# Kernel tuning notes

Measured on AMD Instinct MI355X. Metric: run time of the kernel, lower is better.

Reference implementation:

```python
import jax, jax.numpy as jnp
import numpy as np

NUM_HEAD = 8
MSA_DIM = 256
PAIR_DIM = 128
KEY_DIM = MSA_DIM // NUM_HEAD  # 32 per-head dim
LN_EPS = 1e-5


def _layernorm(x, scale, offset):
    mu = jnp.mean(x, axis=-1, keepdims=True)
    var = jnp.var(x, axis=-1, keepdims=True)
    return (x - mu) * jax.lax.rsqrt(var + LN_EPS) * scale + offset


def setup_inputs() -> dict:
    key = jax.random.key(0)
    ks = jax.random.split(key, 16)
    S, R = 256, 256  # num sequences, num residues
    inp = {
        "msa_act": jax.random.normal(ks[0], (S, R, MSA_DIM), dtype=jnp.float32),
        "msa_mask": jnp.ones((S, R), dtype=jnp.int32),
        "pair_act": jax.random.normal(ks[1], (R, R, PAIR_DIM), dtype=jnp.float32),
        # LayerNorm params
        "qn_scale": jax.random.normal(ks[2], (MSA_DIM,), dtype=jnp.float32) * 0.02 + 1.0,
        "qn_offset": jax.random.normal(ks[3], (MSA_DIM,), dtype=jnp.float32) * 0.02,
        "pn_scale": jax.random.normal(ks[4], (PAIR_DIM,), dtype=jnp.float32) * 0.02 + 1.0,
        "pn_offset": jax.random.normal(ks[5], (PAIR_DIM,), dtype=jnp.float32) * 0.02,
        # pair-bias projection
        "feat_2d_weights": jax.random.normal(ks[6], (PAIR_DIM, NUM_HEAD), dtype=jnp.float32) * 0.1,
        # attention params
        "q_weights": jax.random.normal(ks[7], (MSA_DIM, NUM_HEAD, KEY_DIM), dtype=jnp.float32) * 0.05,
        "k_weights": jax.random.normal(ks[8], (MSA_DIM, NUM_HEAD, KEY_DIM), dtype=jnp.float32) * 0.05,
        "v_weights": jax.random.normal(ks[9], (MSA_DIM, NUM_HEAD, KEY_DIM), dtype=jnp.float32) * 0.05,
        "o_weights": jax.random.normal(ks[10], (NUM_HEAD, KEY_DIM, MSA_DIM), dtype=jnp.float32) * 0.05,
        "o_bias": jnp.zeros((MSA_DIM,), dtype=jnp.float32),
        "gating_w": jax.random.normal(ks[11], (MSA_DIM, NUM_HEAD, KEY_DIM), dtype=jnp.float32) * 0.05,
        "gating_b": jnp.ones((NUM_HEAD, KEY_DIM), dtype=jnp.float32),
    }
    return inp


def reference(msa_act, msa_mask, pair_act, qn_scale, qn_offset, pn_scale, pn_offset,
              feat_2d_weights, q_weights, k_weights, v_weights, o_weights, o_bias,
              gating_w, gating_b):
    # mask bias: [S, 1, 1, R]
    bias = (1e9 * (msa_mask.astype(jnp.float32) - 1.0))[:, None, None, :]
    m = _layernorm(msa_act, qn_scale, qn_offset)            # [S, R, C]
    p = _layernorm(pair_act, pn_scale, pn_offset)           # [R, R, Cz]
    nonbatched_bias = jnp.einsum('qkc,ch->hqk', p, feat_2d_weights)  # [H, R, R]

    q = jnp.einsum('bqa,ahc->bqhc', m, q_weights) * (KEY_DIM ** -0.5)
    k = jnp.einsum('bka,ahc->bkhc', m, k_weights)
    v = jnp.einsum('bka,ahc->bkhc', m, v_weights)
    logits = jnp.einsum('bqhc,bkhc->bhqk', q, k) + bias + nonbatched_bias[None]
    weights = jax.nn.softmax(logits, axis=-1)
    weighted_avg = jnp.einsum('bhqk,bkhc->bqhc', weights, v)

    gate = jax.nn.sigmoid(jnp.einsum('bqc,chv->bqhv', m, gating_w) + gating_b)
    weighted_avg = weighted_avg * gate

    out = jnp.einsum('bqhc,hco->bqo', weighted_avg, o_weights) + o_bias
    return out
```

## Files before the change

kernel.cpp:

```cpp
#include <hip/hip_runtime.h>
#include <hip/hip_bf16.h>
#include <stdint.h>


typedef unsigned short u16;
typedef unsigned int   u32;
typedef __attribute__((ext_vector_type(8))) short bf16x8;
typedef __attribute__((ext_vector_type(4))) float f32x4;

__device__ __forceinline__ float bf2f(u16 u){ union { u32 i; float f; } v; v.i = ((u32)u)<<16; return v.f; }
__device__ __forceinline__ u16 f2bf(float f){
  union { float f; u32 i; } v; v.f = f; u32 x = v.i;
  return (u16)((x + 0x7fffu + ((x>>16)&1u)) >> 16);
}
__device__ __forceinline__ u32 pk2(float a, float b){ return (u32)f2bf(a) | ((u32)f2bf(b) << 16); }

__device__ __forceinline__ void gl_lds16(const void* g, void* l){
  __builtin_amdgcn_global_load_lds(
    reinterpret_cast<const __attribute__((address_space(1))) unsigned int*>(reinterpret_cast<uintptr_t>(g)),
    reinterpret_cast<__attribute__((address_space(3))) unsigned int*>(reinterpret_cast<uintptr_t>(l)),
    16, 0, 0);
}

__global__ __launch_bounds__(256) void k_ln_msa(
    const float* __restrict__ x, const float* __restrict__ sc,
    const float* __restrict__ of, u16* __restrict__ mo)
{
  const int lane = threadIdx.x & 63;
  const int row  = (blockIdx.x << 2) + (threadIdx.x >> 6);
  float4 v = ((const float4*)(x + (size_t)row * 256))[lane];
  float s  = v.x + v.y + v.z + v.w;
  float s2 = v.x*v.x + v.y*v.y + v.z*v.z + v.w*v.w;
  #pragma unroll
  for (int o = 32; o > 0; o >>= 1){ s += __shfl_xor(s, o); s2 += __shfl_xor(s2, o); }
  const float mu = s * (1.0f/256.0f);
  const float rs = rsqrtf(s2 * (1.0f/256.0f) - mu*mu + 1e-5f);
  float4 scv = ((const float4*)sc)[lane];
  float4 ofv = ((const float4*)of)[lane];
  u32 p0 = pk2((v.x-mu)*rs*scv.x + ofv.x, (v.y-mu)*rs*scv.y + ofv.y);
  u32 p1 = pk2((v.z-mu)*rs*scv.z + ofv.z, (v.w-mu)*rs*scv.w + ofv.w);
  ((uint2*)(mo + (size_t)row * 256))[lane] = make_uint2(p0, p1);
}

__global__ __launch_bounds__(256) void k_ln_pair(
    const float* __restrict__ p, const float* __restrict__ sc,
    const float* __restrict__ of, const float* __restrict__ w2d,
    float* __restrict__ nb)
{
  const int lane = threadIdx.x & 63;
  const int row  = (blockIdx.x << 2) + (threadIdx.x >> 6);
  float2 v = ((const float2*)(p + (size_t)row * 128))[lane];
  float s = v.x + v.y, s2 = v.x*v.x + v.y*v.y;
  #pragma unroll
  for (int o = 32; o > 0; o >>= 1){ s += __shfl_xor(s, o); s2 += __shfl_xor(s2, o); }
  const float mu = s * (1.0f/128.0f);
  const float rs = rsqrtf(s2 * (1.0f/128.0f) - mu*mu + 1e-5f);
  const int c0 = lane * 2;
  const float y0 = (v.x - mu) * rs * sc[c0]     + of[c0];
  const float y1 = (v.y - mu) * rs * sc[c0 + 1] + of[c0 + 1];
  const float4* w0 = (const float4*)(w2d + c0 * 8);
  const float4* w1 = (const float4*)(w2d + (c0 + 1) * 8);
  float4 a0 = w0[0], b0 = w0[1], a1 = w1[0], b1 = w1[1];
  float ph[8];
  ph[0] = y0*a0.x + y1*a1.x; ph[1] = y0*a0.y + y1*a1.y;
  ph[2] = y0*a0.z + y1*a1.z; ph[3] = y0*a0.w + y1*a1.w;
  ph[4] = y0*b0.x + y1*b1.x; ph[5] = y0*b0.y + y1*b1.y;
  ph[6] = y0*b0.z + y1*b1.z; ph[7] = y0*b0.w + y1*b1.w;
  #pragma unroll
  for (int o = 32; o > 0; o >>= 1){
    #pragma unroll
    for (int hh = 0; hh < 8; hh++) ph[hh] += __shfl_xor(ph[hh], o);
  }
  if (lane == 0){
    #pragma unroll
    for (int hh = 0; hh < 8; hh++) nb[(size_t)hh * 65536 + row] = ph[hh];
  }
}

__global__ __launch_bounds__(256) void k_cast(
    const float* __restrict__ qw, const float* __restrict__ kw,
    const float* __restrict__ vw, const float* __restrict__ gw,
    const float* __restrict__ ow, u16* __restrict__ wT)
{
  const int mt = blockIdx.x >> 4;
  const float* src = (mt == 0) ? qw : (mt == 1) ? kw : (mt == 2) ? vw : (mt == 3) ? gw : ow;
  u16* dst = wT + mt * 65536;
  const int tid = threadIdx.x;
  const int n  = ((blockIdx.x & 15) << 4) + (tid & 15);
  const int kc = tid >> 4;
  float v[16];
  #pragma unroll
  for (int kk = 0; kk < 16; kk++) v[kk] = src[(kc*16 + kk)*256 + n];
  #pragma unroll
  for (int p = 0; p < 8; p++)
    *(u32*)&dst[n*256 + kc*16 + 2*p] = pk2(v[2*p], v[2*p+1]);
}

__global__ __launch_bounds__(256) void k_qkvg(
    const u16* __restrict__ m, const u16* __restrict__ wT, const float* __restrict__ gb,
    u16* __restrict__ qo, u16* __restrict__ ko, u16* __restrict__ vTo, u16* __restrict__ go)
{
  __shared__ __align__(16) u16 As[8192];
  __shared__ __align__(16) u16 Bs[8192];
  const int tid = threadIdx.x;
  const int w = tid >> 6, lane = tid & 63, g = lane >> 4, q16 = lane & 15;
  const int by = blockIdx.x & 7, bx = blockIdx.x >> 3;
  const int row0  = bx << 7;
  const int mat   = by >> 1;
  const int ncol0 = (by & 1) << 7;
  const u16* Wt = wT + mat * 65536;
  const int wr = w >> 1, wc = w & 1;

  const int rA  = ((tid >> 7) << 4) + (tid & 15);
  const int kgA = (tid >> 4) & 7;

  const f32x4 z4 = {0.f, 0.f, 0.f, 0.f};
  f32x4 acc[4][4];
  #pragma unroll
  for (int i = 0; i < 4; i++)
    #pragma unroll
    for (int j = 0; j < 4; j++) acc[i][j] = z4;

  #pragma unroll 1
  for (int ks = 0; ks < 4; ks++){
    const int k0 = ks << 6;
    #pragma unroll
    for (int c = 0; c < 4; c++){
      gl_lds16(m  + (size_t)(row0  + rA + c*32)*256 + k0 + kgA*8,
               (char*)As + c*4096 + w*1024);
      gl_lds16(Wt + (size_t)(ncol0 + rA + c*32)*256 + k0 + kgA*8,
               (char*)Bs + c*4096 + w*1024);
    }
    __syncthreads();
    #pragma unroll
    for (int kk = 0; kk < 2; kk++){
      bf16x8 af[4], bfr[4];
      #pragma unroll
      for (int i = 0; i < 4; i++){
        af[i]  = *(const bf16x8*)((const char*)As + (wr*4+i)*2048 + (kk*4+g)*256 + q16*16);
        bfr[i] = *(const bf16x8*)((const char*)Bs + (wc*4+i)*2048 + (kk*4+g)*256 + q16*16);
      }
      #pragma unroll
      for (int i = 0; i < 4; i++)
        #pragma unroll
        for (int j = 0; j < 4; j++)
          acc[i][j] = __builtin_amdgcn_mfma_f32_16x16x32_bf16(af[i], bfr[j], acc[i][j], 0, 0, 0);
    }
    __syncthreads();
  }

  const int b  = bx >> 1;
  const int rb = (row0 & 255) + wr*64 + 4*g;
  const int cb0 = ncol0 + wc*64 + q16;

  if (mat == 2){
    #pragma unroll
    for (int i = 0; i < 4; i++){
      const int r = rb + i*16;
      #pragma unroll
      for (int j = 0; j < 4; j++){
        const int col = cb0 + j*16;
        const int hh = col >> 5, cc = col & 31;
        u16* base = vTo + (size_t)(b*8 + hh)*8192 + cc*256 + r;
        *(u32*)base       = pk2(acc[i][j][0], acc[i][j][1]);
        *(u32*)(base + 2) = pk2(acc[i][j][2], acc[i][j][3]);
      }
    }
  } else {
    u16* O = (mat == 0) ? qo : (mat == 1) ? ko : go;
    #pragma unroll
    for (int i = 0; i < 4; i++){
      #pragma unroll
      for (int j = 0; j < 4; j++){
        const int col = cb0 + j*16;
        const int hh = col >> 5, cc = col & 31;
        f32x4 a = acc[i][j];
        if (mat == 0) a *= 0.17677669529663687f;
        #pragma unroll
        for (int v = 0; v < 4; v++){
          float x = a[v];
          if (mat == 3) x = 1.0f / (1.0f + __expf(-(x + gb[col])));
          O[(size_t)((b*8 + hh)*256 + rb + i*16 + v)*32 + cc] = f2bf(x);
        }
      }
    }
  }
}

__global__ __launch_bounds__(512, 4) void k_attn(
    const u16* __restrict__ qp, const u16* __restrict__ kp, const u16* __restrict__ vTp,
    const u16* __restrict__ gp, const int* __restrict__ mask, const float* __restrict__ nb,
    u16* __restrict__ gwa)
{
  __shared__ __align__(16) u16 Ksh[8192];
  __shared__ __align__(16) u16 Vsh[8192];
  __shared__ __align__(16) u16 Pb[8][2048];
  __shared__ float maskb[256];
  const int tid = threadIdx.x;
  const int w = tid >> 6, lane = tid & 63, g = lane >> 4, q16 = lane & 15;
  const int blk = blockIdx.x, b = blk >> 3, h = blk & 7;
  const size_t tb = (size_t)blk * 8192;

  #pragma unroll
  for (int c = 0; c < 2; c++){
    gl_lds16(kp  + tb + (size_t)((c*8 + w)*16 + q16)*32 + g*8,
             (char*)Ksh + c*8192 + w*1024);
    gl_lds16(vTp + tb + (size_t)(c*16 + q16)*256 + (w*4 + g)*8,
             (char*)Vsh + c*8192 + w*1024);
  }
  if (tid < 256) maskb[tid] = 1e9f * ((float)mask[b*256 + tid] - 1.0f);
  __syncthreads();

  const float* nbh = nb + (size_t)h * 65536;
  const f32x4 z4 = {0.f,0.f,0.f,0.f};
  u16* pb = Pb[w];
  const int rsw = (g ^ (q16 & 3)) << 4;

  #pragma unroll 1
  for (int jj = 0; jj < 2; jj++){
    const int q = w*32 + jj*16 + q16;
    const bf16x8 qf = *(const bf16x8*)(qp + tb + (size_t)q*32 + g*8);
    f32x4 O0 = z4, O1 = z4;
    float l = 0.f, mrun = -3.0e38f;

    #pragma unroll 1
    for (int hh = 0; hh < 2; hh++){
      f32x4 S[8];
      #pragma unroll
      for (int n8 = 0; n8 < 8; n8++){
        const bf16x8 kf = *(const bf16x8*)((const char*)Ksh + (hh*8+n8)*1024 + g*256 + q16*16);
        S[n8] = __builtin_amdgcn_mfma_f32_16x16x32_bf16(kf, qf, z4, 0, 0, 0);
      }
      float hmax = -3.0e38f;
      #pragma unroll
      for (int n8 = 0; n8 < 8; n8++){
        const f32x4 nbv = *(const f32x4*)(nbh + (size_t)q*256 + (hh*8+n8)*16 + 4*g);
        const f32x4 mbv = *(const f32x4*)&maskb[(hh*8+n8)*16 + 4*g];
        S[n8] += nbv + mbv;
        hmax = fmaxf(hmax, fmaxf(fmaxf(S[n8][0],S[n8][1]), fmaxf(S[n8][2],S[n8][3])));
      }
      hmax = fmaxf(hmax, __shfl_xor(hmax, 16));
      hmax = fmaxf(hmax, __shfl_xor(hmax, 32));
      const float mnew = fmaxf(mrun, hmax);
      const float fsc = __expf(mrun - mnew);
      l *= fsc; O0 *= fsc; O1 *= fsc; mrun = mnew;

      u32 cpk[8], dpk[8];
      #pragma unroll
      for (int n8 = 0; n8 < 8; n8++){
        const float p0 = __expf(S[n8][0]-mnew), p1 = __expf(S[n8][1]-mnew);
        const float p2 = __expf(S[n8][2]-mnew), p3 = __expf(S[n8][3]-mnew);
        l += (p0+p1)+(p2+p3);
        cpk[n8] = pk2(p0,p1); dpk[n8] = pk2(p2,p3);
      }
      #pragma unroll
      for (int n8 = 0; n8 < 8; n8++){
        const int sl = (2*(n8&1) + (g>>1)) ^ (q16&3);
        *(uint2*)((char*)pb + (n8>>1)*1024 + q16*64 + sl*16 + (g&1)*8)
            = make_uint2(cpk[n8], dpk[n8]);
      }
      #pragma unroll
      for (int c4 = 0; c4 < 4; c4++){
        const bf16x8 pf = *(const bf16x8*)((const char*)pb + c4*1024 + q16*64 + rsw);
        const int kg = (hh*4 + c4)*4 + g;
        const bf16x8 v0 = *(const bf16x8*)((const char*)Vsh + kg*256 + q16*16);
        const bf16x8 v1 = *(const bf16x8*)((const char*)Vsh + 8192 + kg*256 + q16*16);
        O0 = __builtin_amdgcn_mfma_f32_16x16x32_bf16(v0, pf, O0, 0, 0, 0);
        O1 = __builtin_amdgcn_mfma_f32_16x16x32_bf16(v1, pf, O1, 0, 0, 0);
      }
    }

    l += __shfl_xor(l, 16);
    l += __shfl_xor(l, 32);
    const float inv = 1.0f / l;

    const uint2 gvA = *(const uint2*)(gp + tb + (size_t)q*32 + 4*g);
    const uint2 gvB = *(const uint2*)(gp + tb + (size_t)q*32 + 16 + 4*g);
    const float ga0 = bf2f((u16)(gvA.x & 0xffffu)), ga1 = bf2f((u16)(gvA.x >> 16));
    const float ga2 = bf2f((u16)(gvA.y & 0xffffu)), ga3 = bf2f((u16)(gvA.y >> 16));
    const float gb0 = bf2f((u16)(gvB.x & 0xffffu)), gb1 = bf2f((u16)(gvB.x >> 16));
    const float gb2 = bf2f((u16)(gvB.y & 0xffffu)), gb3 = bf2f((u16)(gvB.y >> 16));
    u16* dst = gwa + (size_t)(b*256 + q)*256 + h*32 + 4*g;
    *(u32*)dst        = pk2(O0[0]*inv*ga0, O0[1]*inv*ga1);
    *(u32*)(dst + 2)  = pk2(O0[2]*inv*ga2, O0[3]*inv*ga3);
    *(u32*)(dst + 16) = pk2(O1[0]*inv*gb0, O1[1]*inv*gb1);
    *(u32*)(dst + 18) = pk2(O1[2]*inv*gb2, O1[3]*inv*gb3);
  }
}

__global__ __launch_bounds__(256) void k_out(
    const u16* __restrict__ a, const u16* __restrict__ Wt, const float* __restrict__ ob,
    float* __restrict__ out)
{
  __shared__ __align__(16) u16 As[8192];
  __shared__ __align__(16) u16 Bs[8192];
  const int tid = threadIdx.x;
  const int w = tid >> 6, lane = tid & 63, g = lane >> 4, q16 = lane & 15;
  const int by = blockIdx.x & 1, bx = blockIdx.x >> 1;
  const int row0  = bx << 7;
  const int ncol0 = by << 7;
  const int wr = w >> 1, wc = w & 1;

  const int rA  = ((tid >> 7) << 4) + (tid & 15);
  const int kgA = (tid >> 4) & 7;

  const f32x4 z4 = {0.f, 0.f, 0.f, 0.f};
  f32x4 acc[4][4];
  #pragma unroll
  for (int i = 0; i < 4; i++)
    #pragma unroll
    for (int j = 0; j < 4; j++) acc[i][j] = z4;

  #pragma unroll 1
  for (int ks = 0; ks < 4; ks++){
    const int k0 = ks << 6;
    #pragma unroll
    for (int c = 0; c < 4; c++){
      gl_lds16(a  + (size_t)(row0  + rA + c*32)*256 + k0 + kgA*8,
               (char*)As + c*4096 + w*1024);
      gl_lds16(Wt + (size_t)(ncol0 + rA + c*32)*256 + k0 + kgA*8,
               (char*)Bs + c*4096 + w*1024);
    }
    __syncthreads();
    #pragma unroll
    for (int kk = 0; kk < 2; kk++){
      bf16x8 af[4], bfr[4];
      #pragma unroll
      for (int i = 0; i < 4; i++){
        af[i]  = *(const bf16x8*)((const char*)As + (wr*4+i)*2048 + (kk*4+g)*256 + q16*16);
        bfr[i] = *(const bf16x8*)((const char*)Bs + (wc*4+i)*2048 + (kk*4+g)*256 + q16*16);
      }
      #pragma unroll
      for (int i = 0; i < 4; i++)
        #pragma unroll
        for (int j = 0; j < 4; j++)
          acc[i][j] = __builtin_amdgcn_mfma_f32_16x16x32_bf16(af[i], bfr[j], acc[i][j], 0, 0, 0);
    }
    __syncthreads();
  }

  const int rb = row0 + wr*64 + 4*g;
  #pragma unroll
  for (int i = 0; i < 4; i++){
    #pragma unroll
    for (int j = 0; j < 4; j++){
      const int col = ncol0 + wc*64 + j*16 + q16;
      const float bias = ob[col];
      #pragma unroll
      for (int v = 0; v < 4; v++)
        out[(size_t)(rb + i*16 + v)*256 + col] = acc[i][j][v] + bias;
    }
  }
}

extern "C" void kernel_launch(void* const* d_in, const int* in_sizes, int n_in,
                              void* d_out, int out_size, void* d_ws, size_t ws_size,
                              hipStream_t stream)
{
  (void)in_sizes; (void)n_in; (void)out_size; (void)ws_size;
  const float* msa  = (const float*)d_in[0];
  const int*   mask = (const int*)  d_in[1];
  const float* pair = (const float*)d_in[2];
  const float* qns  = (const float*)d_in[3];
  const float* qno  = (const float*)d_in[4];
  const float* pns  = (const float*)d_in[5];
  const float* pno  = (const float*)d_in[6];
  const float* w2d  = (const float*)d_in[7];
  const float* qw   = (const float*)d_in[8];
  const float* kw   = (const float*)d_in[9];
  const float* vw   = (const float*)d_in[10];
  const float* ow   = (const float*)d_in[11];
  const float* ob   = (const float*)d_in[12];
  const float* gw   = (const float*)d_in[13];
  const float* gb   = (const float*)d_in[14];
  float* out = (float*)d_out;

  char* ws = (char*)d_ws;
  u16*   m_ws = (u16*)ws;
  float* nb   = (float*)(ws + 33554432);
  u16*   q_ws = (u16*)(ws + 35651584);
  u16*   k_ws = q_ws + 16777216;
  u16*   vT_ws= k_ws + 16777216;
  u16*   g_ws = vT_ws + 16777216;
  u16*   wT   = (u16*)(ws + 169869312);
  u16*   gwa  = m_ws;

  k_ln_msa <<<16384, 256, 0, stream>>>(msa, qns, qno, m_ws);
  k_ln_pair<<<16384, 256, 0, stream>>>(pair, pns, pno, w2d, nb);
  k_cast   <<<   80, 256, 0, stream>>>(qw, kw, vw, gw, ow, wT);
  k_qkvg   <<< 4096, 256, 0, stream>>>(m_ws, wT, gb, q_ws, k_ws, vT_ws, g_ws);
  k_attn   <<< 2048, 512, 0, stream>>>(q_ws, k_ws, vT_ws, g_ws, mask, nb, gwa);
  k_out    <<< 1024, 256, 0, stream>>>(gwa, wT + 4*65536, ob, out);
}
```

Before: 489.4 us.

## Double-buffer LDS tiles in projection GEMMs and remap block order

Both the QKVG projection GEMM and the output-projection GEMM now use two LDS buffers. The global-to-LDS load for the next K slice is issued before the MFMAs on the current slice, and one barrier per iteration is dropped. Block indices are also remapped so that consecutive blocks cover 8 row tiles sharing one weight column tile, which aims to improve cache reuse. This doubles LDS use per block, which may lower occupancy.

```diff
diff --git a/kernel.cpp b/kernel.cpp
--- a/kernel.cpp
+++ b/kernel.cpp
@@ -100,11 +100,13 @@
     const u16* __restrict__ m, const u16* __restrict__ wT, const float* __restrict__ gb,
     u16* __restrict__ qo, u16* __restrict__ ko, u16* __restrict__ vTo, u16* __restrict__ go)
 {
-  __shared__ __align__(16) u16 As[8192];
-  __shared__ __align__(16) u16 Bs[8192];
+  __shared__ __align__(16) u16 As[2][8192];
+  __shared__ __align__(16) u16 Bs[2][8192];
   const int tid = threadIdx.x;
   const int w = tid >> 6, lane = tid & 63, g = lane >> 4, q16 = lane & 15;
-  const int by = blockIdx.x & 7, bx = blockIdx.x >> 3;
+  const int blk = blockIdx.x;
+  const int bx = ((blk >> 6) << 3) | (blk & 7);
+  const int by = (blk >> 3) & 7;
   const int row0  = bx << 7;
   const int mat   = by >> 1;
   const int ncol0 = (by & 1) << 7;
@@ -121,24 +123,33 @@
     #pragma unroll
     for (int j = 0; j < 4; j++) acc[i][j] = z4;
 
+  auto STAGE = [&](int buf, int ks){
+    const int k0 = ks << 6;
+    #pragma unroll
+    for (int c = 0; c < 4; c++){
+      gl_lds16(m  + (size_t)(row0  + rA + c*32)*256 + k0 + kgA*8,
+               (char*)As + buf*16384 + c*4096 + w*1024);
+      gl_lds16(Wt + (size_t)(ncol0 + rA + c*32)*256 + k0 + kgA*8,
+               (char*)Bs + buf*16384 + c*4096 + w*1024);
+    }
+  };
+
+  STAGE(0, 0);
+  __syncthreads();
+
   #pragma unroll 1
   for (int ks = 0; ks < 4; ks++){
-    const int k0 = ks << 6;
-    #pragma unroll
-    for (int c = 0; c < 4; c++){
-      gl_lds16(m  + (size_t)(row0  + rA + c*32)*256 + k0 + kgA*8,
-               (char*)As + c*4096 + w*1024);
-      gl_lds16(Wt + (size_t)(ncol0 + rA + c*32)*256 + k0 + kgA*8,
-               (char*)Bs + c*4096 + w*1024);
-    }
-    __syncthreads();
+    const int cur = ks & 1;
+    if (ks < 3) STAGE(cur ^ 1, ks + 1);
+    const char* Ab = (const char*)As + cur*16384;
+    const char* Bb = (const char*)Bs + cur*16384;
     #pragma unroll
     for (int kk = 0; kk < 2; kk++){
       bf16x8 af[4], bfr[4];
       #pragma unroll
       for (int i = 0; i < 4; i++){
-        af[i]  = *(const bf16x8*)((const char*)As + (wr*4+i)*2048 + (kk*4+g)*256 + q16*16);
-        bfr[i] = *(const bf16x8*)((const char*)Bs + (wc*4+i)*2048 + (kk*4+g)*256 + q16*16);
+        af[i]  = *(const bf16x8*)(Ab + (wr*4+i)*2048 + (kk*4+g)*256 + q16*16);
+        bfr[i] = *(const bf16x8*)(Bb + (wc*4+i)*2048 + (kk*4+g)*256 + q16*16);
       }
       #pragma unroll
       for (int i = 0; i < 4; i++)
@@ -146,7 +157,7 @@
         for (int j = 0; j < 4; j++)
           acc[i][j] = __builtin_amdgcn_mfma_f32_16x16x32_bf16(af[i], bfr[j], acc[i][j], 0, 0, 0);
     }
-    __syncthreads();
+    if (ks < 3) __syncthreads();
   }
 
   const int b  = bx >> 1;
@@ -292,11 +303,13 @@
     const u16* __restrict__ a, const u16* __restrict__ Wt, const float* __restrict__ ob,
     float* __restrict__ out)
 {
-  __shared__ __align__(16) u16 As[8192];
-  __shared__ __align__(16) u16 Bs[8192];
+  __shared__ __align__(16) u16 As[2][8192];
+  __shared__ __align__(16) u16 Bs[2][8192];
   const int tid = threadIdx.x;
   const int w = tid >> 6, lane = tid & 63, g = lane >> 4, q16 = lane & 15;
-  const int by = blockIdx.x & 1, bx = blockIdx.x >> 1;
+  const int blk = blockIdx.x;
+  const int bx = ((blk >> 4) << 3) | (blk & 7);
+  const int by = (blk >> 3) & 1;
   const int row0  = bx << 7;
   const int ncol0 = by << 7;
   const int wr = w >> 1, wc = w & 1;
@@ -311,24 +324,33 @@
     #pragma unroll
     for (int j = 0; j < 4; j++) acc[i][j] = z4;
 
+  auto STAGE = [&](int buf, int ks){
+    const int k0 = ks << 6;
+    #pragma unroll
+    for (int c = 0; c < 4; c++){
+      gl_lds16(a  + (size_t)(row0  + rA + c*32)*256 + k0 + kgA*8,
+               (char*)As + buf*16384 + c*4096 + w*1024);
+      gl_lds16(Wt + (size_t)(ncol0 + rA + c*32)*256 + k0 + kgA*8,
+               (char*)Bs + buf*16384 + c*4096 + w*1024);
+    }
+  };
+
+  STAGE(0, 0);
+  __syncthreads();
+
   #pragma unroll 1
   for (int ks = 0; ks < 4; ks++){
-    const int k0 = ks << 6;
-    #pragma unroll
-    for (int c = 0; c < 4; c++){
-      gl_lds16(a  + (size_t)(row0  + rA + c*32)*256 + k0 + kgA*8,
-               (char*)As + c*4096 + w*1024);
-      gl_lds16(Wt + (size_t)(ncol0 + rA + c*32)*256 + k0 + kgA*8,
-               (char*)Bs + c*4096 + w*1024);
-    }
-    __syncthreads();
+    const int cur = ks & 1;
+    if (ks < 3) STAGE(cur ^ 1, ks + 1);
+    const char* Ab = (const char*)As + cur*16384;
+    const char* Bb = (const char*)Bs + cur*16384;
     #pragma unroll
     for (int kk = 0; kk < 2; kk++){
       bf16x8 af[4], bfr[4];
       #pragma unroll
       for (int i = 0; i < 4; i++){
-        af[i]  = *(const bf16x8*)((const char*)As + (wr*4+i)*2048 + (kk*4+g)*256 + q16*16);
-        bfr[i] = *(const bf16x8*)((const char*)Bs + (wc*4+i)*2048 + (kk*4+g)*256 + q16*16);
+        af[i]  = *(const bf16x8*)(Ab + (wr*4+i)*2048 + (kk*4+g)*256 + q16*16);
+        bfr[i] = *(const bf16x8*)(Bb + (wc*4+i)*2048 + (kk*4+g)*256 + q16*16);
       }
       #pragma unroll
       for (int i = 0; i < 4; i++)
@@ -336,7 +358,7 @@
         for (int j = 0; j < 4; j++)
           acc[i][j] = __builtin_amdgcn_mfma_f32_16x16x32_bf16(af[i], bfr[j], acc[i][j], 0, 0, 0);
     }
-    __syncthreads();
+    if (ks < 3) __syncthreads();
   }
 
   const int rb = row0 + wr*64 + 4*g;
```

After: 440.2 us. -10.0%, faster.
